# Kernel optimization log

Measured on AMD Instinct MI355X. Metric: run time of the kernel, lower is better.

Reference implementation:

```python
import jax, jax.numpy as jnp
import numpy as np

SEQ, B, N, F_IN = 128, 32, 1024, 16
NHID, G_FEAT, H = 2, 4, 256


def setup_inputs() -> dict:
    key = jax.random.key(0)
    ks = jax.random.split(key, 14)
    inp = {}
    inp['x'] = jax.random.normal(ks[0], (SEQ, B, N, F_IN), jnp.float32)
    # row-scaled random dense adjacency (keeps activations well-conditioned)
    inp['adj'] = jax.random.uniform(ks[1], (N, N), jnp.float32) * (1.0 / N)
    inp['gc1_w'] = jax.random.normal(ks[2], (F_IN, NHID), jnp.float32) * 0.3
    inp['gc1_b'] = jax.random.normal(ks[3], (NHID,), jnp.float32) * 0.1
    inp['gc2_w'] = jax.random.normal(ks[4], (NHID, G_FEAT), jnp.float32) * 0.3
    inp['gc2_b'] = jax.random.normal(ks[5], (G_FEAT,), jnp.float32) * 0.1
    in0 = G_FEAT * N  # GRU layer-0 input size = G_feat * num_nodes
    inp['w_ih_l0'] = jax.random.normal(ks[6], (3 * H, in0), jnp.float32) * 0.02
    inp['w_hh_l0'] = jax.random.normal(ks[7], (3 * H, H), jnp.float32) * 0.05
    inp['b_ih_l0'] = jax.random.normal(ks[8], (3 * H,), jnp.float32) * 0.05
    inp['b_hh_l0'] = jax.random.normal(ks[9], (3 * H,), jnp.float32) * 0.05
    inp['w_ih_l1'] = jax.random.normal(ks[10], (3 * H, H), jnp.float32) * 0.05
    inp['w_hh_l1'] = jax.random.normal(ks[11], (3 * H, H), jnp.float32) * 0.05
    inp['b_ih_l1'] = jax.random.normal(ks[12], (3 * H,), jnp.float32) * 0.05
    inp['b_hh_l1'] = jax.random.normal(ks[13], (3 * H,), jnp.float32) * 0.05
    return inp


def gru_layer(x_seq, h0, w_ih, w_hh, b_ih, b_hh):
    # torch nn.GRU gate math, gate order (r, z, n)
    def step(h, x_t):
        gi = x_t @ w_ih.T + b_ih          # (B, 3H)
        gh = h @ w_hh.T + b_hh            # (B, 3H)
        i_r, i_z, i_n = jnp.split(gi, 3, axis=-1)
        h_r, h_z, h_n = jnp.split(gh, 3, axis=-1)
        r = jax.nn.sigmoid(i_r + h_r)
        z = jax.nn.sigmoid(i_z + h_z)
        n = jnp.tanh(i_n + r * h_n)
        h_new = (1.0 - z) * n + z * h
        return h_new, h_new
    hT, out = jax.lax.scan(step, h0, x_seq)
    return out, hT


def reference(x, adj, gc1_w, gc1_b, gc2_w, gc2_b,
              w_ih_l0, w_hh_l0, b_ih_l0, b_hh_l0,
              w_ih_l1, w_hh_l1, b_ih_l1, b_hh_l1):
    # GCN, vectorized over (seq, batch). GraphConvolution: adj @ (x @ W) + b
    s = jnp.einsum('sbnf,fh->sbnh', x, gc1_w) + gc1_b
    s = jnp.einsum('mn,sbnh->sbmh', adj, s)
    s = jax.nn.relu(s)
    # dropout inactive in eval mode
    s = jnp.einsum('sbnh,hg->sbng', s, gc2_w) + gc2_b
    s = jnp.einsum('mn,sbng->sbmg', adj, s)
    s = jax.nn.log_softmax(s, axis=2)  # dim=1 of per-step (B, N, G) == node axis
    out = s.reshape(SEQ, B, N * G_FEAT)  # .view(batch, -1) per step, stacked
    h0 = jnp.zeros((B, H), out.dtype)
    out, h1 = gru_layer(out, h0, w_ih_l0, w_hh_l0, b_ih_l0, b_hh_l0)
    out, h2 = gru_layer(out, h0, w_ih_l1, w_hh_l1, b_ih_l1, b_hh_l1)
    hn = jnp.stack([h1, h2])  # (n_layers, B, H)
    return out, hn
```

## Files before the change

kernel.cpp:

```cpp
#include <hip/hip_runtime.h>
#include <stdint.h>

constexpr int SEQL = 128;
constexpr int BAT  = 32;
constexpr int NN   = 1024;
constexpr int FIN  = 16;
constexpr int HH   = 256;
constexpr int PQ   = SEQL * BAT;
constexpr float LSM_SHIFT = 6.9314718055994531f;

using f32x4 = __attribute__((ext_vector_type(4))) float;
using s16x8 = __attribute__((ext_vector_type(8))) short;
using u32x4 = __attribute__((ext_vector_type(4))) unsigned int;

__device__ __forceinline__ unsigned short f2bf(float x) {
  unsigned u = __float_as_uint(x);
  u += 0x7fffu + ((u >> 16) & 1u);
  return (unsigned short)(u >> 16);
}
__device__ __forceinline__ float sigm(float x) { return 1.f / (1.f + __expf(-x)); }

__device__ __forceinline__ void gl_lds16(const void* g, void* l) {
  __builtin_amdgcn_global_load_lds(
      (const __attribute__((address_space(1))) void*)g,
      (__attribute__((address_space(3))) void*)l, 16, 0, 0);
}

#if __has_builtin(__builtin_amdgcn_fdot2_f32_bf16)
typedef __bf16 bf16x2_t __attribute__((ext_vector_type(2)));
__device__ __forceinline__ float dot2bf(unsigned w, unsigned h, float acc) {
  return __builtin_amdgcn_fdot2_f32_bf16(__builtin_bit_cast(bf16x2_t, w),
                                         __builtin_bit_cast(bf16x2_t, h), acc, false);
}
#else
__device__ __forceinline__ float dot2bf(unsigned w, unsigned h, float acc) {
  acc += __uint_as_float(w << 16) * __uint_as_float(h << 16);
  acc += __uint_as_float(w & 0xffff0000u) * __uint_as_float(h & 0xffff0000u);
  return acc;
}
#endif

__global__ __launch_bounds__(256) void k1_xw1(const float* __restrict__ x,
    const float* __restrict__ w1, const float* __restrict__ b1,
    unsigned short* __restrict__ Yt) {
  int idx = blockIdx.x * 256 + threadIdx.x;
  int p = idx >> 10, n = idx & 1023;
  const float* xp = x + (size_t)idx * FIN;
  float xv[16];
  *(float4*)(xv + 0)  = *(const float4*)(xp + 0);
  *(float4*)(xv + 4)  = *(const float4*)(xp + 4);
  *(float4*)(xv + 8)  = *(const float4*)(xp + 8);
  *(float4*)(xv + 12) = *(const float4*)(xp + 12);
  float y0 = b1[0], y1 = b1[1];
#pragma unroll
  for (int f = 0; f < 16; ++f) { y0 += xv[f] * w1[2*f]; y1 += xv[f] * w1[2*f+1]; }
  Yt[(size_t)(2*p)   * NN + n] = f2bf(y0);
  Yt[(size_t)(2*p+1) * NN + n] = f2bf(y1);
}

__global__ __launch_bounds__(256) void k_cvt(const float* __restrict__ in,
    unsigned short* __restrict__ out, int n4) {
  int i = blockIdx.x * 256 + threadIdx.x;
  if (i >= n4) return;
  float4 v = *(const float4*)(in + (size_t)i * 4);
  ushort4 o;
  o.x = f2bf(v.x); o.y = f2bf(v.y); o.z = f2bf(v.z); o.w = f2bf(v.w);
  *(ushort4*)(out + (size_t)i * 4) = o;
}

__global__ __launch_bounds__(256) void k_biasadj(const float* __restrict__ wih0,
    const float* __restrict__ bih0, float* __restrict__ biasAdj) {
  int wid = threadIdx.x >> 6, lane = threadIdx.x & 63;
  int j = blockIdx.x * 4 + wid;
  const float* row = wih0 + (size_t)j * 4096;
  float s = 0.f;
  for (int k = lane * 4; k < 4096; k += 256) {
    float4 v = *(const float4*)(row + k);
    s += v.x + v.y + v.z + v.w;
  }
#pragma unroll
  for (int off = 32; off >= 1; off >>= 1) s += __shfl_xor(s, off);
  if (lane == 0) biasAdj[j] = bih0[j] - LSM_SHIFT * s;
}

__global__ __launch_bounds__(256) void k_prep(const float* __restrict__ W,
    unsigned* __restrict__ Wp) {
  int tid = blockIdx.x * 256 + threadIdx.x;
  int j = tid >> 7, k2 = tid & 127;
  float2 wv = *(const float2*)(W + (size_t)j * 256 + 2 * k2);
  unsigned pk = (unsigned)f2bf(wv.x) | ((unsigned)f2bf(wv.y) << 16);
  int i = j >> 8, jg = j & 255, kg = k2 >> 6, c = (k2 >> 2) & 15, u = k2 & 3;
  Wp[(((i * 2 + kg) * 16 + c) << 10) + (jg << 2) + u] = pk;
}

template <int EPI>
__global__ __launch_bounds__(256) void gemm_bt(
    const unsigned short* __restrict__ A, const unsigned short* __restrict__ B,
    void* __restrict__ Cout, const float* __restrict__ bias, int K, int ldc) {
  __shared__ __align__(16) unsigned short As[128 * 64];
  __shared__ __align__(16) unsigned short Bs[128 * 64];
  const int tid = threadIdx.x;
  const int lane = tid & 63, wave = tid >> 6;
  const int ln15 = lane & 15, hi4 = lane >> 4;
  const int wr = wave >> 1, wc = wave & 1;
  const int m0 = blockIdx.y * 128, n0 = blockIdx.x * 128;
  const int rsub = lane >> 3, csub = lane & 7;

  f32x4 acc[4][4];
#pragma unroll
  for (int i = 0; i < 4; ++i)
#pragma unroll
    for (int j = 0; j < 4; ++j) acc[i][j] = {0.f, 0.f, 0.f, 0.f};

  for (int kt = 0; kt < K; kt += 64) {
    __syncthreads();
#pragma unroll
    for (int j = 0; j < 4; ++j) {
      int qq = wave * 4 + j;
      const unsigned short* ga = A + (size_t)(m0 + qq*8 + rsub) * K + kt + csub*8;
      gl_lds16(ga, &As[qq * 512]);
      const unsigned short* gb = B + (size_t)(n0 + qq*8 + rsub) * K + kt + csub*8;
      gl_lds16(gb, &Bs[qq * 512]);
    }
    __syncthreads();
#pragma unroll
    for (int kk = 0; kk < 2; ++kk) {
      s16x8 af[4], bfr[4];
#pragma unroll
      for (int mi = 0; mi < 4; ++mi)
        af[mi] = *(const s16x8*)&As[(wr*64 + mi*16 + ln15) * 64 + kk*32 + hi4*8];
#pragma unroll
      for (int ni = 0; ni < 4; ++ni)
        bfr[ni] = *(const s16x8*)&Bs[(wc*64 + ni*16 + ln15) * 64 + kk*32 + hi4*8];
#pragma unroll
      for (int mi = 0; mi < 4; ++mi)
#pragma unroll
        for (int ni = 0; ni < 4; ++ni)
          acc[mi][ni] = __builtin_amdgcn_mfma_f32_16x16x32_bf16(
              af[mi], bfr[ni], acc[mi][ni], 0, 0, 0);
    }
  }

  if (EPI == 2) {
    float* C = (float*)Cout;
#pragma unroll
    for (int ni = 0; ni < 4; ++ni) {
      int j = n0 + wc*64 + ni*16 + ln15;
      float bv = bias[j];
#pragma unroll
      for (int mi = 0; mi < 4; ++mi) {
        int m = m0 + wr*64 + mi*16 + hi4*4;
#pragma unroll
        for (int r = 0; r < 4; ++r) C[(size_t)(m + r) * ldc + j] = acc[mi][ni][r] + bv;
      }
    }
  } else {
    unsigned short* C = (unsigned short*)Cout;
#pragma unroll
    for (int ni = 0; ni < 4; ++ni) {
      int j = n0 + wc*64 + ni*16 + ln15;
#pragma unroll
      for (int mi = 0; mi < 4; ++mi) {
        int m = m0 + wr*64 + mi*16 + hi4*4;
        ushort4 v;
        float f0 = acc[mi][ni][0], f1 = acc[mi][ni][1], f2 = acc[mi][ni][2], f3 = acc[mi][ni][3];
        if (EPI == 0) { f0 = fmaxf(f0, 0.f); f1 = fmaxf(f1, 0.f); f2 = fmaxf(f2, 0.f); f3 = fmaxf(f3, 0.f); }
        v.x = f2bf(f0); v.y = f2bf(f1); v.z = f2bf(f2); v.w = f2bf(f3);
        *(ushort4*)&C[(size_t)j * ldc + m] = v;
      }
    }
  }
}

__device__ __forceinline__ unsigned k4_proc(unsigned a, unsigned b, float w0, float w1, float bb) {
  float a0 = __uint_as_float(a << 16), a1 = __uint_as_float(a & 0xffff0000u);
  float b0 = __uint_as_float(b << 16), b1 = __uint_as_float(b & 0xffff0000u);
  float y0 = a0 * w0 + b0 * w1 + bb;
  float y1 = a1 * w0 + b1 * w1 + bb;
  return (unsigned)f2bf(y0) | ((unsigned)f2bf(y1) << 16);
}

__global__ __launch_bounds__(256) void k4_w2(const unsigned short* __restrict__ z1t,
    const float* __restrict__ w2, const float* __restrict__ b2,
    unsigned short* __restrict__ Y2t) {
  int idx = blockIdx.x * 256 + threadIdx.x;
  int j4 = idx >> 7, mb = idx & 127;
  int p = j4 >> 2, g = j4 & 3;
  const unsigned short* r0 = z1t + (size_t)(p * 2) * NN + mb * 8;
  const unsigned short* r1 = r0 + NN;
  float w0 = w2[g], w1v = w2[4 + g], bb = b2[g];
  uint4 ua = *(const uint4*)r0;
  uint4 ub = *(const uint4*)r1;
  uint4 o;
  o.x = k4_proc(ua.x, ub.x, w0, w1v, bb);
  o.y = k4_proc(ua.y, ub.y, w0, w1v, bb);
  o.z = k4_proc(ua.z, ub.z, w0, w1v, bb);
  o.w = k4_proc(ua.w, ub.w, w0, w1v, bb);
  *(uint4*)(Y2t + (size_t)j4 * NN + mb * 8) = o;
}

__global__ __launch_bounds__(256) void k6_lsm(const unsigned short* __restrict__ z2t,
    unsigned short* __restrict__ Xg) {
  int wid = threadIdx.x >> 6, lane = threadIdx.x & 63;
  int r = blockIdx.x * 4 + wid;
  int p = r >> 2, g = r & 3;
  const unsigned short* row = z2t + (size_t)r * NN;
  uint4 u0 = *(const uint4*)(row + lane * 16);
  uint4 u1 = *(const uint4*)(row + lane * 16 + 8);
  unsigned uu[8] = {u0.x, u0.y, u0.z, u0.w, u1.x, u1.y, u1.z, u1.w};
  float v[16];
#pragma unroll
  for (int q = 0; q < 8; ++q) {
    v[2*q]   = __uint_as_float(uu[q] << 16);
    v[2*q+1] = __uint_as_float(uu[q] & 0xffff0000u);
  }
  float mx = v[0];
#pragma unroll
  for (int e = 1; e < 16; ++e) mx = fmaxf(mx, v[e]);
#pragma unroll
  for (int off = 32; off >= 1; off >>= 1) mx = fmaxf(mx, __shfl_xor(mx, off));
  float s = 0.f;
#pragma unroll
  for (int e = 0; e < 16; ++e) s += __expf(v[e] - mx);
#pragma unroll
  for (int off = 32; off >= 1; off >>= 1) s += __shfl_xor(s, off);
  float lse = __logf(s) + mx;
  unsigned short* xr = Xg + (size_t)p * 4096;
#pragma unroll
  for (int e = 0; e < 16; ++e) xr[(lane * 16 + e) * 4 + g] = f2bf(v[e] - lse + LSM_SHIFT);
}

template <int L>
__global__ __launch_bounds__(512, 1) void k_rnn(const float* __restrict__ gi,
    const unsigned* __restrict__ Wp, const float* __restrict__ bhh,
    unsigned short* __restrict__ hb_out, float* __restrict__ hf_out,
    float* __restrict__ hn_row) {
  const int b = blockIdx.x, tid = threadIdx.x;
  const int jg = tid & 255, kg = tid >> 8;
  __shared__ __align__(16) unsigned hpk[128];
  __shared__ float part[2][776];

  unsigned w[3][16][4];
#pragma unroll
  for (int i = 0; i < 3; ++i)
#pragma unroll
    for (int c = 0; c < 16; ++c) {
      u32x4 t = *(const u32x4*)(Wp + ((((i * 2 + kg) * 16 + c) << 10) + (jg << 2)));
      w[i][c][0] = t.x; w[i][c][1] = t.y; w[i][c][2] = t.z; w[i][c][3] = t.w;
    }
#pragma unroll
  for (int i = 0; i < 3; ++i)
#pragma unroll
    for (int c = 0; c < 16; ++c)
#pragma unroll
      for (int u = 0; u < 4; ++u)
        asm volatile("" : "+v"(w[i][c][u]));

  float hprev = 0.f;
  float br = 0.f, bz = 0.f, bn = 0.f;
  float g0 = 0.f, g1 = 0.f, g2 = 0.f;
  if (tid < 256) {
    br = bhh[jg]; bz = bhh[256 + jg]; bn = bhh[512 + jg];
    const float* gr = gi + (size_t)(0 * BAT + b) * 768;
    g0 = gr[jg]; g1 = gr[256 + jg]; g2 = gr[512 + jg];
  }
  if (tid < 128) hpk[tid] = 0u;
  __syncthreads();

  for (int t = 0; t < SEQL; ++t) {
    float p0 = 0.f, p1 = 0.f, p2 = 0.f;
    if (tid < 256) {
      int tt = t + 1 < SEQL ? t + 1 : SEQL - 1;
      const float* gr = gi + (size_t)(tt * BAT + b) * 768;
      p0 = gr[jg]; p1 = gr[256 + jg]; p2 = gr[512 + jg];
    }
    float a0 = 0.f, a1 = 0.f, a2 = 0.f;
#pragma unroll
    for (int c = 0; c < 16; ++c) {
      u32x4 hk = *(const u32x4*)&hpk[kg * 64 + c * 4];
      a0 = dot2bf(w[0][c][0], hk.x, a0); a0 = dot2bf(w[0][c][1], hk.y, a0);
      a0 = dot2bf(w[0][c][2], hk.z, a0); a0 = dot2bf(w[0][c][3], hk.w, a0);
      a1 = dot2bf(w[1][c][0], hk.x, a1); a1 = dot2bf(w[1][c][1], hk.y, a1);
      a1 = dot2bf(w[1][c][2], hk.z, a1); a1 = dot2bf(w[1][c][3], hk.w, a1);
      a2 = dot2bf(w[2][c][0], hk.x, a2); a2 = dot2bf(w[2][c][1], hk.y, a2);
      a2 = dot2bf(w[2][c][2], hk.z, a2); a2 = dot2bf(w[2][c][3], hk.w, a2);
    }
    part[kg][jg]       = a0;
    part[kg][256 + jg] = a1;
    part[kg][512 + jg] = a2;
    __syncthreads();
    if (tid < 256) {
      float ghr = part[0][jg]       + part[1][jg]       + br;
      float ghz = part[0][256 + jg] + part[1][256 + jg] + bz;
      float ghn = part[0][512 + jg] + part[1][512 + jg] + bn;
      float r = sigm(g0 + ghr);
      float z = sigm(g1 + ghz);
      float nn = tanhf(g2 + r * ghn);
      float hnew = (1.f - z) * nn + z * hprev;
      hprev = hnew;
      unsigned short hbb = f2bf(hnew);
      if (L == 0) hb_out[(size_t)(t * BAT + b) * 256 + jg] = hbb;
      else        hf_out[(size_t)(t * BAT + b) * 256 + jg] = hnew;
      unsigned lo = (unsigned)hbb;
      unsigned hi = (unsigned)__shfl_down((int)lo, 1);
      if (!(jg & 1)) hpk[jg >> 1] = lo | (hi << 16);
      if (t == SEQL - 1) hn_row[b * 256 + jg] = hnew;
    }
    g0 = p0; g1 = p1; g2 = p2;
    __syncthreads();
  }
}

extern "C" void kernel_launch(void* const* d_in, const int* in_sizes, int n_in,
                              void* d_out, int out_size, void* d_ws, size_t ws_size,
                              hipStream_t stream) {
  const float* x    = (const float*)d_in[0];
  const float* adj  = (const float*)d_in[1];
  const float* gc1w = (const float*)d_in[2];
  const float* gc1b = (const float*)d_in[3];
  const float* gc2w = (const float*)d_in[4];
  const float* gc2b = (const float*)d_in[5];
  const float* wih0 = (const float*)d_in[6];
  const float* whh0 = (const float*)d_in[7];
  const float* bih0 = (const float*)d_in[8];
  const float* bhh0 = (const float*)d_in[9];
  const float* wih1 = (const float*)d_in[10];
  const float* whh1 = (const float*)d_in[11];
  const float* bih1 = (const float*)d_in[12];
  const float* bhh1 = (const float*)d_in[13];

  char* ws = (char*)d_ws;
  const size_t MB = 1048576;
  unsigned short* adjb  = (unsigned short*)(ws + 0);
  unsigned short* Yt    = (unsigned short*)(ws + 2 * MB);
  unsigned short* z1t   = (unsigned short*)(ws + 18 * MB);
  unsigned short* Y2t   = (unsigned short*)(ws + 34 * MB);
  unsigned short* z2t   = (unsigned short*)(ws + 2 * MB);
  unsigned short* Xg    = (unsigned short*)(ws + 34 * MB);
  unsigned short* wih0b = (unsigned short*)(ws + 2 * MB);
  float* biasAdj        = (float*)(ws + 9 * MB);
  float* gi0            = (float*)(ws + 10 * MB);
  unsigned* Whh0p       = (unsigned*)(ws + 23 * MB);
  unsigned* Whh1p       = (unsigned*)(ws + 24 * MB);
  unsigned short* wih1b = (unsigned short*)(ws + 25 * MB);
  unsigned short* h0b   = (unsigned short*)(ws + 25 * MB + 512 * 1024);
  float* gi1            = (float*)(ws + 28 * MB);
  float* out = (float*)d_out;
  float* hn  = out + (size_t)SEQL * BAT * HH;

  k1_xw1<<<PQ * NN / 256, 256, 0, stream>>>(x, gc1w, gc1b, Yt);
  k_cvt<<<(NN * NN / 4 + 255) / 256, 256, 0, stream>>>(adj, adjb, NN * NN / 4);
  gemm_bt<0><<<dim3(64, 8), 256, 0, stream>>>(adjb, Yt, (void*)z1t, nullptr, 1024, 1024);
  k4_w2<<<16384 * 128 / 256, 256, 0, stream>>>(z1t, gc2w, gc2b, Y2t);
  gemm_bt<1><<<dim3(128, 8), 256, 0, stream>>>(adjb, Y2t, (void*)z2t, nullptr, 1024, 1024);
  k6_lsm<<<16384 / 4, 256, 0, stream>>>(z2t, Xg);
  k_biasadj<<<192, 256, 0, stream>>>(wih0, bih0, biasAdj);
  k_cvt<<<(768 * 4096 / 4 + 255) / 256, 256, 0, stream>>>(wih0, wih0b, 768 * 4096 / 4);
  gemm_bt<2><<<dim3(6, 32), 256, 0, stream>>>(Xg, wih0b, (void*)gi0, biasAdj, 4096, 768);
  k_prep<<<384, 256, 0, stream>>>(whh0, Whh0p);
  k_prep<<<384, 256, 0, stream>>>(whh1, Whh1p);
  k_cvt<<<(768 * 256 / 4 + 255) / 256, 256, 0, stream>>>(wih1, wih1b, 768 * 256 / 4);
  k_rnn<0><<<32, 512, 0, stream>>>(gi0, Whh0p, bhh0, h0b, nullptr, hn);
  gemm_bt<2><<<dim3(6, 32), 256, 0, stream>>>(h0b, wih1b, (void*)gi1, bih1, 256, 768);
  k_rnn<1><<<32, 512, 0, stream>>>(gi1, Whh1p, bhh1, nullptr, out, hn + BAT * HH);
}
```

Measured before the change: 655.5 us.

## Split GRU recurrent dot products across four K-groups with 1024-thread blocks

The recurrent GRU kernel now splits the hidden-dimension reduction into four K-groups instead of two, launching 1024 threads per batch block, each holding half as many packed bf16 weights in registers. Partial sums are stored interleaved so the gate thread reads them with one float4 load per gate, and the next h chunk is prefetched from LDS while the current one is used. This shortens each thread's serial dot-product chain per timestep, which is the latency-bound critical path, at the cost of more threads per barrier and a wider cross-wave reduction.

```diff
diff --git a/kernel.cpp b/kernel.cpp
--- a/kernel.cpp
+++ b/kernel.cpp
@@ -89,8 +89,8 @@
   int j = tid >> 7, k2 = tid & 127;
   float2 wv = *(const float2*)(W + (size_t)j * 256 + 2 * k2);
   unsigned pk = (unsigned)f2bf(wv.x) | ((unsigned)f2bf(wv.y) << 16);
-  int i = j >> 8, jg = j & 255, kg = k2 >> 6, c = (k2 >> 2) & 15, u = k2 & 3;
-  Wp[(((i * 2 + kg) * 16 + c) << 10) + (jg << 2) + u] = pk;
+  int i = j >> 8, jg = j & 255, kg = k2 >> 5, c = (k2 >> 2) & 7, u = k2 & 3;
+  Wp[((((i * 4 + kg) * 8 + c)) << 10) + (jg << 2) + u] = pk;
 }
 
 template <int EPI>
@@ -231,37 +231,32 @@
 }
 
 template <int L>
-__global__ __launch_bounds__(512, 1) void k_rnn(const float* __restrict__ gi,
+__global__ __launch_bounds__(1024) void k_rnn(const float* __restrict__ gi,
     const unsigned* __restrict__ Wp, const float* __restrict__ bhh,
     unsigned short* __restrict__ hb_out, float* __restrict__ hf_out,
     float* __restrict__ hn_row) {
   const int b = blockIdx.x, tid = threadIdx.x;
   const int jg = tid & 255, kg = tid >> 8;
   __shared__ __align__(16) unsigned hpk[128];
-  __shared__ float part[2][776];
-
-  unsigned w[3][16][4];
+  __shared__ __align__(16) float part2[768 * 4];
+
+  unsigned w[3][8][4];
 #pragma unroll
   for (int i = 0; i < 3; ++i)
 #pragma unroll
-    for (int c = 0; c < 16; ++c) {
-      u32x4 t = *(const u32x4*)(Wp + ((((i * 2 + kg) * 16 + c) << 10) + (jg << 2)));
+    for (int c = 0; c < 8; ++c) {
+      u32x4 t = *(const u32x4*)(Wp + ((((i * 4 + kg) * 8 + c) << 10) + (jg << 2)));
       w[i][c][0] = t.x; w[i][c][1] = t.y; w[i][c][2] = t.z; w[i][c][3] = t.w;
-    }
-#pragma unroll
-  for (int i = 0; i < 3; ++i)
-#pragma unroll
-    for (int c = 0; c < 16; ++c)
-#pragma unroll
-      for (int u = 0; u < 4; ++u)
-        asm volatile("" : "+v"(w[i][c][u]));
+#pragma unroll
+      for (int u = 0; u < 4; ++u) asm volatile("" : "+v"(w[i][c][u]));
+    }
 
   float hprev = 0.f;
   float br = 0.f, bz = 0.f, bn = 0.f;
   float g0 = 0.f, g1 = 0.f, g2 = 0.f;
   if (tid < 256) {
     br = bhh[jg]; bz = bhh[256 + jg]; bn = bhh[512 + jg];
-    const float* gr = gi + (size_t)(0 * BAT + b) * 768;
+    const float* gr = gi + (size_t)b * 768;
     g0 = gr[jg]; g1 = gr[256 + jg]; g2 = gr[512 + jg];
   }
   if (tid < 128) hpk[tid] = 0u;
@@ -275,24 +270,29 @@
       p0 = gr[jg]; p1 = gr[256 + jg]; p2 = gr[512 + jg];
     }
     float a0 = 0.f, a1 = 0.f, a2 = 0.f;
-#pragma unroll
-    for (int c = 0; c < 16; ++c) {
-      u32x4 hk = *(const u32x4*)&hpk[kg * 64 + c * 4];
+    u32x4 hk = *(const u32x4*)&hpk[kg * 32];
+#pragma unroll
+    for (int c = 0; c < 8; ++c) {
+      u32x4 hnx = (c < 7) ? *(const u32x4*)&hpk[kg * 32 + (c + 1) * 4] : hk;
       a0 = dot2bf(w[0][c][0], hk.x, a0); a0 = dot2bf(w[0][c][1], hk.y, a0);
       a0 = dot2bf(w[0][c][2], hk.z, a0); a0 = dot2bf(w[0][c][3], hk.w, a0);
       a1 = dot2bf(w[1][c][0], hk.x, a1); a1 = dot2bf(w[1][c][1], hk.y, a1);
       a1 = dot2bf(w[1][c][2], hk.z, a1); a1 = dot2bf(w[1][c][3], hk.w, a1);
       a2 = dot2bf(w[2][c][0], hk.x, a2); a2 = dot2bf(w[2][c][1], hk.y, a2);
       a2 = dot2bf(w[2][c][2], hk.z, a2); a2 = dot2bf(w[2][c][3], hk.w, a2);
-    }
-    part[kg][jg]       = a0;
-    part[kg][256 + jg] = a1;
-    part[kg][512 + jg] = a2;
+      hk = hnx;
+    }
+    part2[(jg << 2) + kg]           = a0;
+    part2[((256 + jg) << 2) + kg]   = a1;
+    part2[((512 + jg) << 2) + kg]   = a2;
     __syncthreads();
     if (tid < 256) {
-      float ghr = part[0][jg]       + part[1][jg]       + br;
-      float ghz = part[0][256 + jg] + part[1][256 + jg] + bz;
-      float ghn = part[0][512 + jg] + part[1][512 + jg] + bn;
+      float4 pr = *(const float4*)&part2[jg << 2];
+      float4 pz = *(const float4*)&part2[(256 + jg) << 2];
+      float4 pn = *(const float4*)&part2[(512 + jg) << 2];
+      float ghr = pr.x + pr.y + pr.z + pr.w + br;
+      float ghz = pz.x + pz.y + pz.z + pz.w + bz;
+      float ghn = pn.x + pn.y + pn.z + pn.w + bn;
       float r = sigm(g0 + ghr);
       float z = sigm(g1 + ghz);
       float nn = tanhf(g2 + r * ghn);
@@ -360,7 +360,7 @@
   k_prep<<<384, 256, 0, stream>>>(whh0, Whh0p);
   k_prep<<<384, 256, 0, stream>>>(whh1, Whh1p);
   k_cvt<<<(768 * 256 / 4 + 255) / 256, 256, 0, stream>>>(wih1, wih1b, 768 * 256 / 4);
-  k_rnn<0><<<32, 512, 0, stream>>>(gi0, Whh0p, bhh0, h0b, nullptr, hn);
+  k_rnn<0><<<32, 1024, 0, stream>>>(gi0, Whh0p, bhh0, h0b, nullptr, hn);
   gemm_bt<2><<<dim3(6, 32), 256, 0, stream>>>(h0b, wih1b, (void*)gi1, bih1, 256, 768);
-  k_rnn<1><<<32, 512, 0, stream>>>(gi1, Whh1p, bhh1, nullptr, out, hn + BAT * HH);
-}
+  k_rnn<1><<<32, 1024, 0, stream>>>(gi1, Whh1p, bhh1, nullptr, out, hn + BAT * HH);
+}
```

Measured after the change: 745.9 us. 13.8% more time.
